# Performance work log

Measured on AMD Instinct MI355X. Metric: run time of the kernel, lower is better.

The kernel has to match this reference:

```python
import jax, jax.numpy as jnp
import numpy as np

MU = 1.0
VUL = 1.0
M = 1.0
ETA = 0.5

BATCH = 256
NBIT = 64
NCLASS = 100
TRAIN_SIZE = 200000


def setup_inputs() -> dict:
    key = jax.random.key(0)
    k1, k2, k3, k4, k5 = jax.random.split(key, 5)
    u = jax.random.normal(k1, (BATCH, NBIT), dtype=jnp.float32)
    labels = jax.random.randint(k2, (BATCH,), 0, NCLASS)
    y = jax.nn.one_hot(labels, NCLASS, dtype=jnp.float32)
    # unique indices into the training-set buffers
    ind = jax.random.permutation(k3, TRAIN_SIZE)[:BATCH]
    U = jax.random.normal(k4, (NBIT, TRAIN_SIZE), dtype=jnp.float32)
    buf_labels = jax.random.randint(k5, (TRAIN_SIZE,), 0, NCLASS)
    Y = jax.nn.one_hot(buf_labels, NCLASS, dtype=jnp.float32).T  # (nclass, train_size)
    C = jnp.sign(jax.random.normal(jax.random.fold_in(key, 7), (NBIT, NCLASS), dtype=jnp.float32))
    return {"u": u, "y": y, "ind": ind, "U": U, "Y": Y, "C": C}


def _discrete_center(C, y, b):
    """Discrete cyclic coordinate descent over class rows. C: (nbit, nclass)."""
    Ct = C.T                      # (nclass, nbit)
    Yt = y.T                      # (nclass, batch)
    Q = Yt @ b.T                  # (nclass, nbit), constant across iterations
    G = Yt @ Yt.T                 # (nclass, nclass) Gram of label rows
    nclass = Ct.shape[0]

    def body(i, Ct):
        w = G[:, i].at[i].set(0.0)          # Y_prime @ v, self row excluded
        colsum = Ct.sum(axis=0) - Ct[i]     # C_prime.T @ ones
        new_row = jnp.sign(Q[i] - Ct.T @ w - VUL * colsum)
        return Ct.at[i].set(new_row)

    Ct = jax.lax.fori_loop(0, nclass, body, Ct)
    return Ct.T  # back to (nbit, nclass)


def reference(u, y, ind, U, Y, C):
    yf = y.astype(jnp.float32)
    # persistent buffer updates (detached in the original via .data)
    U_new = U.at[:, ind].set(jax.lax.stop_gradient(u.T))
    Y_new = Y.at[:, ind].set(yf.T)
    # binary targets for this batch
    b = jax.lax.stop_gradient(jnp.sign(MU * (C @ yf.T) + u.T))  # (nbit, batch)
    # DCC update of class centers (runs under no_grad in the original)
    C_new = _discrete_center(jax.lax.stop_gradient(C), jax.lax.stop_gradient(yf), b)
    # pairwise similarity loss against the whole training buffer
    s = (yf @ Y_new > 0).astype(u.dtype)                 # (batch, train_size)
    ip = jnp.clip(u @ U_new * 0.5, -100.0, 50.0)          # (batch, train_size)
    metric_loss = jnp.mean((1.0 - s) * jnp.log1p(jnp.exp(M + ip))
                           + s * jnp.log1p(jnp.exp(M - ip)))
    quantization_loss = jnp.mean((b - u.T) ** 2)
    loss = metric_loss + ETA * quantization_loss
    return loss, C_new
```

## Files before the change

### kernel.cpp

```cpp
#include <hip/hip_runtime.h>
#include <hip/hip_bf16.h>

#define T_TOTAL 200000
#define BATCH 256
#define NBIT 64
#define NCLASS 100
#define TN 128
#define NBLK ((T_TOTAL + TN - 1) / TN)

typedef __attribute__((ext_vector_type(8))) short bf16x8;
typedef __attribute__((ext_vector_type(4))) float f32x4;

#define LOG2E 1.4426950408889634f
#define LN2   0.6931471805599453

__device__ __forceinline__ float sgnf(float v) {
    return (v > 0.f) ? 1.f : ((v < 0.f) ? -1.f : 0.f);
}

__device__ __forceinline__ unsigned int pk2(float a, float b) {
    union { __hip_bfloat162 h2; unsigned int ui; } cv;
    cv.h2 = __float22bfloat162_rn(make_float2(a, b));
    return cv.ui;
}

__global__ __launch_bounds__(256) void prep_kernel(const float* __restrict__ u,
                                                   const float* __restrict__ y,
                                                   int* __restrict__ labB,
                                                   unsigned short* __restrict__ Abf) {
    const int gt = blockIdx.x * 256 + threadIdx.x;
    {
        const int f = gt * 2;
        const int row = f >> 4, p = f & 15;
        const float4* up = reinterpret_cast<const float4*>(u);
        float4 a = up[f], b = up[f + 1];
        uint4 w = make_uint4(pk2(0.5f * a.x, 0.5f * a.y), pk2(0.5f * a.z, 0.5f * a.w),
                             pk2(0.5f * b.x, 0.5f * b.y), pk2(0.5f * b.z, 0.5f * b.w));
        *reinterpret_cast<uint4*>(&Abf[row * 64 + p * 4]) = w;
    }
    if (gt < BATCH) {
        const float4* yp = reinterpret_cast<const float4*>(y + gt * NCLASS);
        int l = 0;
        #pragma unroll
        for (int p = 0; p < 25; ++p) {
            float4 v = yp[p];
            if (v.x > 0.5f) l = p * 4;
            if (v.y > 0.5f) l = p * 4 + 1;
            if (v.z > 0.5f) l = p * 4 + 2;
            if (v.w > 0.5f) l = p * 4 + 3;
        }
        labB[gt] = l;
    }
}

__global__ __launch_bounds__(256) void laby_kernel(const float* __restrict__ Y,
                                                   int* __restrict__ lab_buf) {
    const unsigned stride = gridDim.x * 256;
    const float4* Y4 = reinterpret_cast<const float4*>(Y);
    for (unsigned q = blockIdx.x * 256 + threadIdx.x; q < 5000000u; q += stride) {
        float4 v = Y4[q];
        unsigned r = q / 50000u;
        unsigned t = (q - r * 50000u) * 4u;
        if (v.x > 0.5f) lab_buf[t]     = (int)r;
        if (v.y > 0.5f) lab_buf[t + 1] = (int)r;
        if (v.z > 0.5f) lab_buf[t + 2] = (int)r;
        if (v.w > 0.5f) lab_buf[t + 3] = (int)r;
    }
}

__global__ __launch_bounds__(256) void dcc_kernel(const float* __restrict__ u,
                                                  const float* __restrict__ C,
                                                  const int* __restrict__ lab,
                                                  float* __restrict__ out_c,
                                                  float* __restrict__ quant_out) {
    __shared__ float Q[NCLASS][NBIT];
    __shared__ float Ct[NCLASS][NBIT];
    __shared__ int   labL[BATCH];
    __shared__ float wq[4];

    const int tid = threadIdx.x;
    const int k   = tid & 63;
    const int g   = tid >> 6;

    labL[tid] = lab[tid];
    for (int o = tid; o < NCLASS * NBIT; o += 256) {
        ((float*)Q)[o] = 0.f;
        int i = o >> 6, kk = o & 63;
        Ct[i][kk] = C[kk * NCLASS + i];
    }
    __syncthreads();

    float qloc = 0.f;
    for (int jj = 0; jj < 64; ++jj) {
        int j = g * 64 + jj;
        int lj = labL[j];
        float uu = u[j * NBIT + k];
        float b = sgnf(Ct[lj][k] + uu);
        atomicAdd(&Q[lj][k], b);
        float d = b - uu;
        qloc += d * d;
    }
    for (int off = 32; off; off >>= 1) qloc += __shfl_xor(qloc, off);
    if ((tid & 63) == 0) wq[g] = qloc;
    __syncthreads();
    if (tid == 0) quant_out[0] = wq[0] + wq[1] + wq[2] + wq[3];

    if (tid < 64) {
        float total = 0.f;
        for (int i = 0; i < NCLASS; ++i) total += Ct[i][k];
        for (int i = 0; i < NCLASS; ++i) {
            float old = Ct[i][k];
            float v = Q[i][k] - (total - old);
            float nr = sgnf(v);
            Ct[i][k] = nr;
            total += nr - old;
        }
    }
    __syncthreads();
    for (int o = tid; o < NCLASS * NBIT; o += 256) {
        int kk = o / NCLASS, i = o - kk * NCLASS;
        out_c[o] = Ct[i][kk];
    }
}

__global__ __launch_bounds__(256, 6) void metric_kernel(const float* __restrict__ u,
                                                        const float* __restrict__ U,
                                                        const int* __restrict__ ind,
                                                        const int* __restrict__ labB_g,
                                                        const int* __restrict__ lab_buf,
                                                        const unsigned short* __restrict__ Abf,
                                                        double* __restrict__ partial) {
    __shared__ unsigned short Bt[TN * 64];
    __shared__ int   labT[TN];
    __shared__ int   labB[BATCH];
    __shared__ float wpart[4];

    const int tid = threadIdx.x;
    const long t0 = (long)blockIdx.x * TN;

    labB[tid] = labB_g[tid];
    if (tid < TN) {
        long t = t0 + tid;
        labT[tid] = (t < (long)T_TOTAL) ? lab_buf[t] : -1;
    }

    {
        const int c = tid & 127;
        const int h = tid >> 7;
        const long t = t0 + c;
        const bool ok = (t < (long)T_TOTAL);
        const int sw = (c & 7) << 3;
        #pragma unroll
        for (int m = 0; m < 4; ++m) {
            unsigned int w[4];
            #pragma unroll
            for (int pp = 0; pp < 4; ++pp) {
                const int kk = h * 32 + m * 8 + 2 * pp;
                float v0 = 0.f, v1 = 0.f;
                if (ok) {
                    v0 = U[(long)kk * T_TOTAL + t];
                    v1 = U[(long)(kk + 1) * T_TOTAL + t];
                }
                w[pp] = pk2(v0, v1);
            }
            const int k0 = h * 32 + m * 8;
            *reinterpret_cast<uint4*>(&Bt[c * 64 + (k0 ^ sw)]) = make_uint4(w[0], w[1], w[2], w[3]);
        }
    }
    __syncthreads();
    {
        long c = (long)ind[tid] - t0;
        if (c >= 0 && c < TN) {
            labT[c] = labB[tid];
            const int ci = (int)c;
            const int sw = (ci & 7) << 3;
            #pragma unroll
            for (int m = 0; m < 8; ++m) {
                unsigned int w[4];
                #pragma unroll
                for (int pp = 0; pp < 4; ++pp) {
                    float v0 = u[tid * NBIT + m * 8 + 2 * pp];
                    float v1 = u[tid * NBIT + m * 8 + 2 * pp + 1];
                    w[pp] = pk2(v0, v1);
                }
                *reinterpret_cast<uint4*>(&Bt[ci * 64 + ((m * 8) ^ sw)]) = make_uint4(w[0], w[1], w[2], w[3]);
            }
        }
    }
    __syncthreads();

    const int wid  = tid >> 6;
    const int lane = tid & 63;
    const int lr   = lane & 15;
    const int g4   = lane >> 4;

    bf16x8 afrag[4][2];
    #pragma unroll
    for (int mt = 0; mt < 4; ++mt) {
        #pragma unroll
        for (int kb = 0; kb < 2; ++kb) {
            const int j = wid * 64 + mt * 16 + lr;
            union { bf16x8 v; uint4 q; } pk;
            pk.q = *reinterpret_cast<const uint4*>(&Abf[j * 64 + kb * 32 + g4 * 8]);
            afrag[mt][kb] = pk.v;
        }
    }
    int labR[4][4];
    #pragma unroll
    for (int mt = 0; mt < 4; ++mt)
        #pragma unroll
        for (int e = 0; e < 4; ++e)
            labR[mt][e] = labB[wid * 64 + mt * 16 + g4 * 4 + e];

    float sum2 = 0.f;
    for (int nt = 0; nt < 8; ++nt) {
        if (t0 + nt * 16 >= (long)T_TOTAL) break;
        const int col = nt * 16 + lr;
        const int sw = (col & 7) << 3;
        union { bf16x8 v; uint4 q; } b0, b1;
        b0.q = *reinterpret_cast<const uint4*>(&Bt[col * 64 + ((g4 * 8) ^ sw)]);
        b1.q = *reinterpret_cast<const uint4*>(&Bt[col * 64 + ((32 + g4 * 8) ^ sw)]);
        const int labc = labT[col];
        #pragma unroll
        for (int mt = 0; mt < 4; ++mt) {
            f32x4 acc4 = {0.f, 0.f, 0.f, 0.f};
            acc4 = __builtin_amdgcn_mfma_f32_16x16x32_bf16(afrag[mt][0], b0.v, acc4, 0, 0, 0);
            acc4 = __builtin_amdgcn_mfma_f32_16x16x32_bf16(afrag[mt][1], b1.v, acc4, 0, 0, 0);
            #pragma unroll
            for (int e = 0; e < 4; ++e) {
                float ip = fminf(fmaxf(acc4[e], -100.f), 50.f);
                float z  = (labc == labR[mt][e]) ? -ip : ip;
                float tt = fmaf(z, LOG2E, LOG2E);
                float e2 = exp2f(tt);
                sum2 += log2f(1.f + e2);
            }
        }
    }
    for (int off = 32; off; off >>= 1) sum2 += __shfl_xor(sum2, off);
    if (lane == 0) wpart[wid] = sum2;
    __syncthreads();
    if (tid == 0)
        partial[blockIdx.x] = (double)(wpart[0] + wpart[1] + wpart[2] + wpart[3]) * LN2;
}

__global__ __launch_bounds__(256) void fin_kernel(const double* __restrict__ partial,
                                                  const float* __restrict__ quant,
                                                  float* __restrict__ out0) {
    __shared__ double wp[4];
    double s = 0.0;
    for (int i = threadIdx.x; i < NBLK; i += 256) s += partial[i];
    for (int off = 32; off; off >>= 1) s += __shfl_xor(s, off);
    if ((threadIdx.x & 63) == 0) wp[threadIdx.x >> 6] = s;
    __syncthreads();
    if (threadIdx.x == 0) {
        double tot = wp[0] + wp[1] + wp[2] + wp[3];
        out0[0] = (float)(tot / ((double)BATCH * (double)T_TOTAL)
                          + 0.5 * ((double)quant[0] / (double)(BATCH * NBIT)));
    }
}

extern "C" void kernel_launch(void* const* d_in, const int* in_sizes, int n_in,
                              void* d_out, int out_size, void* d_ws, size_t ws_size,
                              hipStream_t stream) {
    const float* u   = (const float*)d_in[0];
    const float* y   = (const float*)d_in[1];
    const int*   ind = (const int*)d_in[2];
    const float* U   = (const float*)d_in[3];
    const float* Y   = (const float*)d_in[4];
    const float* C   = (const float*)d_in[5];
    float* out = (float*)d_out;

    float*          quant   = (float*)d_ws;
    int*            labB    = (int*)((char*)d_ws + 64);
    unsigned short* Abf     = (unsigned short*)((char*)d_ws + 2048);
    double*         partial = (double*)((char*)d_ws + 36864);
    int*            lab_buf = (int*)((char*)d_ws + 65536);

    prep_kernel<<<8, 256, 0, stream>>>(u, y, labB, Abf);
    laby_kernel<<<2048, 256, 0, stream>>>(Y, lab_buf);
    dcc_kernel<<<1, 256, 0, stream>>>(u, C, labB, out + 1, quant);
    metric_kernel<<<NBLK, 256, 0, stream>>>(u, U, ind, labB, lab_buf, Abf, partial);
    fin_kernel<<<1, 256, 0, stream>>>(partial, quant, out);
}
```

Before: 277.6 us.

## Fuse label prep kernels, use raw hw exp/log, transpose-free DCC layout

Merges the prep and Y-label scan kernels into one launch whose grid is split by row, so the per-element divide in the scan goes away. The metric kernel's softplus now calls the raw v_exp_f32/v_log_f32 instructions instead of exp2f/log2f, skipping their range and denormal handling. The DCC kernel keeps C in its native (nbit, nclass) layout, which removes the transposed load and store, and prefetches the next Q and Ct values in the serial sweep. Raw hardware log and exp may differ slightly in accuracy near edge values.

```diff
diff --git a/kernel.cpp b/kernel.cpp
--- a/kernel.cpp
+++ b/kernel.cpp
@@ -7,6 +7,7 @@
 #define NCLASS 100
 #define TN 128
 #define NBLK ((T_TOTAL + TN - 1) / TN)
+#define YBLK 196
 
 typedef __attribute__((ext_vector_type(8))) short bf16x8;
 typedef __attribute__((ext_vector_type(4))) float f32x4;
@@ -24,47 +25,56 @@
     return cv.ui;
 }
 
-__global__ __launch_bounds__(256) void prep_kernel(const float* __restrict__ u,
-                                                   const float* __restrict__ y,
-                                                   int* __restrict__ labB,
-                                                   unsigned short* __restrict__ Abf) {
-    const int gt = blockIdx.x * 256 + threadIdx.x;
-    {
-        const int f = gt * 2;
-        const int row = f >> 4, p = f & 15;
-        const float4* up = reinterpret_cast<const float4*>(u);
-        float4 a = up[f], b = up[f + 1];
-        uint4 w = make_uint4(pk2(0.5f * a.x, 0.5f * a.y), pk2(0.5f * a.z, 0.5f * a.w),
-                             pk2(0.5f * b.x, 0.5f * b.y), pk2(0.5f * b.z, 0.5f * b.w));
-        *reinterpret_cast<uint4*>(&Abf[row * 64 + p * 4]) = w;
-    }
-    if (gt < BATCH) {
-        const float4* yp = reinterpret_cast<const float4*>(y + gt * NCLASS);
-        int l = 0;
-        #pragma unroll
-        for (int p = 0; p < 25; ++p) {
-            float4 v = yp[p];
-            if (v.x > 0.5f) l = p * 4;
-            if (v.y > 0.5f) l = p * 4 + 1;
-            if (v.z > 0.5f) l = p * 4 + 2;
-            if (v.w > 0.5f) l = p * 4 + 3;
-        }
-        labB[gt] = l;
-    }
-}
-
-__global__ __launch_bounds__(256) void laby_kernel(const float* __restrict__ Y,
-                                                   int* __restrict__ lab_buf) {
-    const unsigned stride = gridDim.x * 256;
-    const float4* Y4 = reinterpret_cast<const float4*>(Y);
-    for (unsigned q = blockIdx.x * 256 + threadIdx.x; q < 5000000u; q += stride) {
-        float4 v = Y4[q];
-        unsigned r = q / 50000u;
-        unsigned t = (q - r * 50000u) * 4u;
-        if (v.x > 0.5f) lab_buf[t]     = (int)r;
-        if (v.y > 0.5f) lab_buf[t + 1] = (int)r;
-        if (v.z > 0.5f) lab_buf[t + 2] = (int)r;
-        if (v.w > 0.5f) lab_buf[t + 3] = (int)r;
+__device__ __forceinline__ float hw_exp2(float x) {
+    float r; asm("v_exp_f32 %0, %1" : "=v"(r) : "v"(x)); return r;
+}
+__device__ __forceinline__ float hw_log2(float x) {
+    float r; asm("v_log_f32 %0, %1" : "=v"(r) : "v"(x)); return r;
+}
+
+__global__ __launch_bounds__(256) void laby_prep_kernel(const float* __restrict__ Y,
+                                                        int* __restrict__ lab_buf,
+                                                        const float* __restrict__ u,
+                                                        const float* __restrict__ y,
+                                                        int* __restrict__ labB,
+                                                        unsigned short* __restrict__ Abf) {
+    const int bid = blockIdx.x;
+    if (bid < YBLK * NCLASS) {
+        const int row = bid / YBLK;
+        const int xb  = bid - row * YBLK;
+        const int t4  = xb * 256 + threadIdx.x;
+        if (t4 < T_TOTAL / 4) {
+            float4 v = reinterpret_cast<const float4*>(Y)[(long)row * (T_TOTAL / 4) + t4];
+            const int t = t4 * 4;
+            if (v.x > 0.5f) lab_buf[t]     = row;
+            if (v.y > 0.5f) lab_buf[t + 1] = row;
+            if (v.z > 0.5f) lab_buf[t + 2] = row;
+            if (v.w > 0.5f) lab_buf[t + 3] = row;
+        }
+    } else {
+        const int gt = (bid - YBLK * NCLASS) * 256 + threadIdx.x;
+        {
+            const int f = gt * 2;
+            const int row = f >> 4, p = f & 15;
+            const float4* up = reinterpret_cast<const float4*>(u);
+            float4 a = up[f], b = up[f + 1];
+            uint4 w = make_uint4(pk2(0.5f * a.x, 0.5f * a.y), pk2(0.5f * a.z, 0.5f * a.w),
+                                 pk2(0.5f * b.x, 0.5f * b.y), pk2(0.5f * b.z, 0.5f * b.w));
+            *reinterpret_cast<uint4*>(&Abf[row * 64 + p * 4]) = w;
+        }
+        if (gt < BATCH) {
+            const float4* yp = reinterpret_cast<const float4*>(y + gt * NCLASS);
+            int l = 0;
+            #pragma unroll
+            for (int p = 0; p < 25; ++p) {
+                float4 v = yp[p];
+                if (v.x > 0.5f) l = p * 4;
+                if (v.y > 0.5f) l = p * 4 + 1;
+                if (v.z > 0.5f) l = p * 4 + 2;
+                if (v.w > 0.5f) l = p * 4 + 3;
+            }
+            labB[gt] = l;
+        }
     }
 }
 
@@ -74,7 +84,7 @@
                                                   float* __restrict__ out_c,
                                                   float* __restrict__ quant_out) {
     __shared__ float Q[NCLASS][NBIT];
-    __shared__ float Ct[NCLASS][NBIT];
+    __shared__ float Ct2[NBIT * NCLASS];
     __shared__ int   labL[BATCH];
     __shared__ float wq[4];
 
@@ -85,8 +95,7 @@
     labL[tid] = lab[tid];
     for (int o = tid; o < NCLASS * NBIT; o += 256) {
         ((float*)Q)[o] = 0.f;
-        int i = o >> 6, kk = o & 63;
-        Ct[i][kk] = C[kk * NCLASS + i];
+        Ct2[o] = C[o];
     }
     __syncthreads();
 
@@ -95,7 +104,7 @@
         int j = g * 64 + jj;
         int lj = labL[j];
         float uu = u[j * NBIT + k];
-        float b = sgnf(Ct[lj][k] + uu);
+        float b = sgnf(Ct2[k * NCLASS + lj] + uu);
         atomicAdd(&Q[lj][k], b);
         float d = b - uu;
         qloc += d * d;
@@ -107,20 +116,18 @@
 
     if (tid < 64) {
         float total = 0.f;
-        for (int i = 0; i < NCLASS; ++i) total += Ct[i][k];
+        for (int i = 0; i < NCLASS; ++i) total += Ct2[k * NCLASS + i];
+        float qn = Q[0][k], cn = Ct2[k * NCLASS];
         for (int i = 0; i < NCLASS; ++i) {
-            float old = Ct[i][k];
-            float v = Q[i][k] - (total - old);
-            float nr = sgnf(v);
-            Ct[i][k] = nr;
+            float qc = qn, old = cn;
+            if (i + 1 < NCLASS) { qn = Q[i + 1][k]; cn = Ct2[k * NCLASS + i + 1]; }
+            float nr = sgnf(qc - (total - old));
+            Ct2[k * NCLASS + i] = nr;
             total += nr - old;
         }
     }
     __syncthreads();
-    for (int o = tid; o < NCLASS * NBIT; o += 256) {
-        int kk = o / NCLASS, i = o - kk * NCLASS;
-        out_c[o] = Ct[i][kk];
-    }
+    for (int o = tid; o < NCLASS * NBIT; o += 256) out_c[o] = Ct2[o];
 }
 
 __global__ __launch_bounds__(256, 6) void metric_kernel(const float* __restrict__ u,
@@ -231,8 +238,7 @@
                 float ip = fminf(fmaxf(acc4[e], -100.f), 50.f);
                 float z  = (labc == labR[mt][e]) ? -ip : ip;
                 float tt = fmaf(z, LOG2E, LOG2E);
-                float e2 = exp2f(tt);
-                sum2 += log2f(1.f + e2);
+                sum2 += hw_log2(1.f + hw_exp2(tt));
             }
         }
     }
@@ -276,8 +282,7 @@
     double*         partial = (double*)((char*)d_ws + 36864);
     int*            lab_buf = (int*)((char*)d_ws + 65536);
 
-    prep_kernel<<<8, 256, 0, stream>>>(u, y, labB, Abf);
-    laby_kernel<<<2048, 256, 0, stream>>>(Y, lab_buf);
+    laby_prep_kernel<<<YBLK * NCLASS + 8, 256, 0, stream>>>(Y, lab_buf, u, y, labB, Abf);
     dcc_kernel<<<1, 256, 0, stream>>>(u, C, labB, out + 1, quant);
     metric_kernel<<<NBLK, 256, 0, stream>>>(u, U, ind, labB, lab_buf, Abf, partial);
     fin_kernel<<<1, 256, 0, stream>>>(partial, quant, out);
```

Result: faster. 271.8 us (-2.1%).
